# Optimization experiments

Hardware: AMD Instinct MI355X
Metric: run time of the kernel (lower is better)

Reference implementation:

```python
import jax, jax.numpy as jnp
import numpy as np

T, B, E, H = 256, 8, 512, 32
EXP = 512            # number of expanded (periodic-image) keys
SMOOTH = 20.0        # smooth_factor


def setup_inputs() -> dict:
    key = jax.random.key(0)
    ks = jax.random.split(key, 12)
    s = 1.0 / np.sqrt(E)
    return {
        "query": jax.random.normal(ks[0], (T, B, E), dtype=jnp.float32),
        "outcell_index": jax.random.randint(ks[1], (B, EXP), 0, T),
        "expand_mask": jax.random.bernoulli(ks[2], 0.1, (B, EXP)),
        "key_padding_mask": jax.random.bernoulli(ks[3], 0.1, (B, T)),
        "local_attention_weight": jax.random.uniform(ks[4], (B, T, T + EXP), dtype=jnp.float32),
        "Wq": jax.random.normal(ks[5], (E, E), dtype=jnp.float32) * s,
        "bq": jnp.zeros((E,), dtype=jnp.float32),
        "Wk": jax.random.normal(ks[6], (E, E), dtype=jnp.float32) * s,   # k_bias=False
        "Wv": jax.random.normal(ks[7], (E, E), dtype=jnp.float32) * s,
        "bv": jnp.zeros((E,), dtype=jnp.float32),
        "Wo": jax.random.normal(ks[8], (E, E), dtype=jnp.float32) * s,
        "bo": jnp.zeros((E,), dtype=jnp.float32),
    }


def reference(query, outcell_index, expand_mask, key_padding_mask,
              local_attention_weight, Wq, bq, Wk, Wv, bv, Wo, bo):
    t, b, e = query.shape
    hd = e // H
    # QKV projections (torch Linear: y = x @ W.T + b)
    q = jnp.einsum('tbe,fe->tbf', query, Wq) + bq
    k = jnp.einsum('tbe,fe->tbf', query, Wk)          # no k bias
    v = jnp.einsum('tbe,fe->tbf', query, Wv) + bv
    # PBC gather-expand K/V along the time axis
    oc = outcell_index.T[:, :, None]                  # [EXP, B, 1]
    k = jnp.concatenate([k, jnp.take_along_axis(k, oc, axis=0)], axis=0)  # [S,B,E]
    v = jnp.concatenate([v, jnp.take_along_axis(v, oc, axis=0)], axis=0)
    s_len = k.shape[0]
    # [len, B, E] -> [B, H, len, hd]
    qh = q.reshape(t, b, H, hd).transpose(1, 2, 0, 3)
    kh = k.reshape(s_len, b, H, hd).transpose(1, 2, 0, 3)
    vh = v.reshape(s_len, b, H, hd).transpose(1, 2, 0, 3)
    # NOTE: forward() never applies self.scaling in this path (faithful)
    scores = jnp.einsum('bhtd,bhsd->bhts', qh, kh)    # [B,H,T,S]
    law = local_attention_weight[:, None]             # [B,1,T,S]
    scores = (scores + SMOOTH) * law - SMOOTH         # smooth softmax
    kpm = jnp.concatenate([key_padding_mask, expand_mask], axis=1)  # [B,S]
    scores = jnp.where(kpm[:, None, None, :], -jnp.inf, scores)
    probs = jax.nn.softmax(scores, axis=-1)
    probs = probs * law                               # post-softmax reweight
    attn = jnp.einsum('bhts,bhsd->bhtd', probs, vh)   # [B,H,T,hd]
    attn = attn.transpose(2, 0, 1, 3).reshape(t, b, e)
    return jnp.einsum('tbe,fe->tbf', attn, Wo) + bo
```

## Files before the change

kernel.cpp:

```cpp
#include <hip/hip_runtime.h>
#include <stdint.h>

#define T_ 256
#define B_ 8
#define E_ 512
#define H_ 32
#define HD_ 16
#define EXP_ 512
#define S_ 768
#define M_ 2048
#define SMOOTH_ 20.0f
#define KSTR 20
#define VSTR 776
#define OSTR 20
#define LOG2E_ 1.44269504f
#define MB0_  (-100.988655f)

typedef __attribute__((ext_vector_type(8)))  short bf16x8;
typedef __attribute__((ext_vector_type(4)))  float f32x4;
typedef __attribute__((ext_vector_type(16))) float f32x16;
typedef __attribute__((ext_vector_type(2)))  unsigned int uint32x2;

__device__ __forceinline__ unsigned int cvtpk(float a, float b)
{
    unsigned int r;
    asm("v_cvt_pk_bf16_f32 %0, %1, %2" : "=v"(r) : "v"(a), "v"(b));
    return r;
}
__device__ __forceinline__ ushort bf1(float a)
{
    unsigned int u = __float_as_uint(a);
    u = u + 0x7FFFu + ((u >> 16) & 1u);
    return (ushort)(u >> 16);
}

union U16 { uint4 u; bf16x8 v; };
union U8x2 { uint2 p[2]; bf16x8 v; };

__device__ __forceinline__ bf16x8 ld20(const ushort* base, int row, int hi)
{
    U8x2 u;
    const ushort* p = &base[row * KSTR + hi * 8];
    u.p[0] = *(const uint2*)(p);
    u.p[1] = *(const uint2*)(p + 4);
    return u.v;
}

__global__ __launch_bounds__(1024, 4)
void qkv_attn_kernel(const float* __restrict__ X,
                     const float* __restrict__ Wq, const float* __restrict__ Wk,
                     const float* __restrict__ Wv,
                     const float* __restrict__ bq, const float* __restrict__ bv,
                     const float* __restrict__ LAW,
                     const int* __restrict__ kpm, const int* __restrict__ em,
                     const int* __restrict__ oc, ushort* __restrict__ Ab)
{
    __shared__ __align__(16) char raw[87552];
    ushort* Ks  = (ushort*)(raw);
    ushort* Vt  = (ushort*)(raw + 30720);
    ushort* Qi  = (ushort*)(raw + 55552);
    float*  msf = (float*) (raw + 65792);
    float*  Obuf= (float*) (raw);
    float*  Zb  = (float*) (raw + 65792);
    ushort* Ob  = Qi;

    const int bh  = blockIdx.x;
    const int b   = bh & 7;
    const int h   = bh >> 3;
    const int tid = threadIdx.x;
    const int w   = tid >> 6;
    const int l   = tid & 63;

    const int r0 = tid >> 3;
    const int c8 = tid & 7;
    const float* Xc0 = &X[((size_t)r0 * 8 + b) * E_ + c8 * 8];
    const float* Xc1 = Xc0 + (size_t)128 * 8 * E_;

    const int wr = tid >> 3;
    const bool wload = (tid < 384);
    const float* Wsel = (wr < 16) ? Wq : (wr < 32 ? Wk : Wv);
    const float* Wr = &Wsel[((size_t)(h * 16 + (wr & 15))) * E_ + c8 * 8];

    f32x4 acc[3];
#pragma unroll
    for (int m = 0; m < 3; ++m) acc[m] = (f32x4){0.f, 0.f, 0.f, 0.f};

    float4 xa0, xa1, xb0, xb1, wp0, wp1;
    xa0 = *(const float4*)&Xc0[0]; xa1 = *(const float4*)&Xc0[4];
    xb0 = *(const float4*)&Xc1[0]; xb1 = *(const float4*)&Xc1[4];
    if (wload) { wp0 = *(const float4*)&Wr[0]; wp1 = *(const float4*)&Wr[4]; }

    const int ln = l & 15;
    const int lg = l >> 4;

    for (int it = 0; it < 8; ++it) {
        ushort* Ad = (ushort*)(raw + (it & 1) * 43776);
        ushort* Bd = Ad + 18432;
        *(uint4*)&Ad[r0 * 72 + c8 * 8] =
            make_uint4(cvtpk(xa0.x, xa0.y), cvtpk(xa0.z, xa0.w),
                       cvtpk(xa1.x, xa1.y), cvtpk(xa1.z, xa1.w));
        *(uint4*)&Ad[(r0 + 128) * 72 + c8 * 8] =
            make_uint4(cvtpk(xb0.x, xb0.y), cvtpk(xb0.z, xb0.w),
                       cvtpk(xb1.x, xb1.y), cvtpk(xb1.z, xb1.w));
        if (wload)
            *(uint4*)&Bd[wr * 72 + c8 * 8] =
                make_uint4(cvtpk(wp0.x, wp0.y), cvtpk(wp0.z, wp0.w),
                           cvtpk(wp1.x, wp1.y), cvtpk(wp1.z, wp1.w));
        __syncthreads();
        if (it < 7) {
            Xc0 += 64; Xc1 += 64;
            xa0 = *(const float4*)&Xc0[0]; xa1 = *(const float4*)&Xc0[4];
            xb0 = *(const float4*)&Xc1[0]; xb1 = *(const float4*)&Xc1[4];
            if (wload) { Wr += 64; wp0 = *(const float4*)&Wr[0]; wp1 = *(const float4*)&Wr[4]; }
        }
#pragma unroll
        for (int kb = 0; kb < 2; ++kb) {
            bf16x8 af = *(const bf16x8*)&Ad[(w * 16 + ln) * 72 + kb * 32 + lg * 8];
#pragma unroll
            for (int m = 0; m < 3; ++m) {
                bf16x8 bfm = *(const bf16x8*)&Bd[(m * 16 + ln) * 72 + kb * 32 + lg * 8];
                acc[m] = __builtin_amdgcn_mfma_f32_16x16x32_bf16(af, bfm, acc[m], 0, 0, 0);
            }
        }
    }

    __syncthreads();

    {
        const float bqv = bq[h * 16 + ln];
        const float bvv = bv[h * 16 + ln];
#pragma unroll
        for (int r = 0; r < 4; ++r) {
            const int t = w * 16 + lg * 4 + r;
            Qi[t * KSTR + ln] = bf1(acc[0][r] + bqv);
            Ks[t * KSTR + ln] = bf1(acc[1][r]);
            Vt[ln * VSTR + t] = bf1(acc[2][r] + bvv);
        }
    }
    __syncthreads();

    if (tid < 512) {
        const int j   = tid;
        const int src = oc[b * EXP_ + j];
        const ushort* sp = &Ks[src * KSTR];
        ushort* dp = &Ks[(T_ + j) * KSTR];
        uint2 k0 = *(const uint2*)(sp);
        uint2 k1 = *(const uint2*)(sp + 4);
        uint2 k2 = *(const uint2*)(sp + 8);
        uint2 k3 = *(const uint2*)(sp + 12);
        uint2 k4 = *(const uint2*)(sp + 16);
        *(uint2*)(dp)      = k0;
        *(uint2*)(dp + 4)  = k1;
        *(uint2*)(dp + 8)  = k2;
        *(uint2*)(dp + 12) = k3;
        *(uint2*)(dp + 16) = k4;
    } else {
        const int j   = tid - 512;
        const int src = oc[b * EXP_ + j];
#pragma unroll
        for (int d = 0; d < 16; ++d)
            Vt[d * VSTR + T_ + j] = Vt[d * VSTR + src];
    }
    if (tid < 768) {
        const int s = tid;
        const int m = (s < T_) ? kpm[b * T_ + s] : em[b * EXP_ + (s - T_)];
        msf[s] = m ? -1.0e5f : MB0_;
    }
    __syncthreads();

    const int slane = l & 31;
    const int hi    = l >> 5;
    const int tq    = w & 7;
    const int sh    = w >> 3;
    const int i0    = sh * 12;
    const int iend  = i0 + 12;

    bf16x8 qf = ld20(Qi, tq * 32 + slane, hi);

    const f32x16 zero16 = {0.f,0.f,0.f,0.f,0.f,0.f,0.f,0.f,
                           0.f,0.f,0.f,0.f,0.f,0.f,0.f,0.f};
    f32x16 oacc = zero16;
    float zp0 = 0.f, zp1 = 0.f, zp2 = 0.f, zp3 = 0.f;

    const float* lawb = &LAW[((size_t)b * T_ + tq * 32 + slane) * S_ + 4 * hi];

    bf16x8 kf = ld20(Ks, i0 * 32 + slane, hi);
    float4 g0 = *(const float4*)&lawb[i0 * 32];
    float4 g1 = *(const float4*)&lawb[i0 * 32 + 8];
    float4 g2 = *(const float4*)&lawb[i0 * 32 + 16];
    float4 g3 = *(const float4*)&lawb[i0 * 32 + 24];

#pragma unroll 2
    for (int i = i0; i < iend; ++i) {
        const int inx = (i + 1 < iend) ? (i + 1) : i0;

        bf16x8 vf0 = *(const bf16x8*)&Vt[(l & 15) * VSTR + i * 32 + hi * 8];
        bf16x8 vf1 = *(const bf16x8*)&Vt[(l & 15) * VSTR + i * 32 + 16 + hi * 8];
        const float4 m0 = *(const float4*)&msf[i * 32 + 4 * hi];
        const float4 m1 = *(const float4*)&msf[i * 32 + 8 + 4 * hi];
        const float4 m2 = *(const float4*)&msf[i * 32 + 16 + 4 * hi];
        const float4 m3 = *(const float4*)&msf[i * 32 + 24 + 4 * hi];

        f32x16 sc = __builtin_amdgcn_mfma_f32_32x32x16_bf16(kf, qf, zero16, 0, 0, 0);

        bf16x8 kfn = ld20(Ks, inx * 32 + slane, hi);

        const float4 lwg[4] = {g0, g1, g2, g3};
        const float4 mbg[4] = {m0, m1, m2, m3};

#pragma unroll
        for (int ks = 0; ks < 2; ++ks) {
            float pp[8];
#pragma unroll
            for (int gi = 0; gi < 2; ++gi) {
                const int g = 2 * ks + gi;
                const float4 lw4 = lwg[g];
                const float4 mb4 = mbg[g];
                const float lwa[4] = {lw4.x, lw4.y, lw4.z, lw4.w};
                const float mba[4] = {mb4.x, mb4.y, mb4.z, mb4.w};
#pragma unroll
                for (int c = 0; c < 4; ++c) {
                    const float lwv = lwa[c];
                    const float lwK = lwv * LOG2E_;
                    const float arg = __builtin_fmaf(sc[8 * ks + 4 * gi + c], lwK,
                                      __builtin_fmaf(lwK, SMOOTH_, mba[c]));
                    const float e = __builtin_amdgcn_exp2f(arg);
                    if (c == 0) zp0 += e; else if (c == 1) zp1 += e;
                    else if (c == 2) zp2 += e; else zp3 += e;
                    pp[4 * gi + c] = e * lwv;
                }
            }
            const unsigned int cA0 = cvtpk(pp[0], pp[1]);
            const unsigned int cA2 = cvtpk(pp[2], pp[3]);
            const unsigned int cB0 = cvtpk(pp[4], pp[5]);
            const unsigned int cB2 = cvtpk(pp[6], pp[7]);
            uint32x2 s0 = __builtin_amdgcn_permlane32_swap(cA0, cB0, false, false);
            uint32x2 s1 = __builtin_amdgcn_permlane32_swap(cA2, cB2, false, false);
            U16 u;
            u.u = make_uint4(s0.x, s1.x, s0.y, s1.y);
            oacc = __builtin_amdgcn_mfma_f32_32x32x16_bf16(
                       u.v, ks ? vf1 : vf0, oacc, 0, 0, 0);
        }

        g0 = *(const float4*)&lawb[inx * 32];
        g1 = *(const float4*)&lawb[inx * 32 + 8];
        g2 = *(const float4*)&lawb[inx * 32 + 16];
        g3 = *(const float4*)&lawb[inx * 32 + 24];
        kf = kfn;
    }

    float z = (zp0 + zp1) + (zp2 + zp3);
    z += __shfl_xor(z, 32);

    __syncthreads();

    if (l < 32) Zb[sh * 256 + tq * 32 + l] = z;

    const int dl = l & 15;
    const bool dok = (l & 31) < 16;
    if (sh == 1 && dok) {
#pragma unroll
        for (int r = 0; r < 16; ++r) {
            const int t = tq * 32 + (r & 3) + 8 * (r >> 2) + 4 * hi;
            Obuf[t * OSTR + dl] = oacc[r];
        }
    }
    __syncthreads();

    if (sh == 0 && dok) {
#pragma unroll
        for (int r = 0; r < 16; ++r) {
            const int t = tq * 32 + (r & 3) + 8 * (r >> 2) + 4 * hi;
            const float Zt  = Zb[t] + Zb[256 + t];
            const float inv = (Zt > 0.f) ? 1.f / Zt : 0.f;
            const float ov  = (oacc[r] + Obuf[t * OSTR + dl]) * inv;
            Ob[t * 16 + dl] = bf1(ov);
        }
    }
    __syncthreads();

    {
        const int t  = tid >> 2;
        const int q4 = tid & 3;
        *(uint2*)&Ab[((size_t)(t * 8 + b)) * E_ + h * 16 + q4 * 4] =
            *(const uint2*)&Ob[t * 16 + q4 * 4];
    }
}

__global__ __launch_bounds__(256, 2)
void out_gemm(const ushort* __restrict__ Ab, const float* __restrict__ Wo,
              const float* __restrict__ bo, float* __restrict__ dst)
{
    __shared__ __align__(16) ushort sbuf[96 * 136];
    ushort* As = sbuf;
    ushort* Bs = sbuf + 32 * 136;

    const int n0 = blockIdx.x * 64;
    const int m0 = blockIdx.y * 32;

    const int tid = threadIdx.x;
    const int arow = tid >> 3;
    const int acol = (tid & 7) * 16;
    const int brow = tid >> 2;
    const int bcol = (tid & 3) * 32;

    const ushort* Ap = &Ab[(size_t)(m0 + arow) * E_ + acol];
    const float*  Wp = &Wo[(size_t)(n0 + brow) * E_ + bcol];

    f32x4 acc[2];
    acc[0] = (f32x4){0.f, 0.f, 0.f, 0.f};
    acc[1] = (f32x4){0.f, 0.f, 0.f, 0.f};

    uint4  ha0 = *(const uint4*)&Ap[0];
    uint4  ha1 = *(const uint4*)&Ap[8];
    float4 f0 = *(const float4*)&Wp[0];
    float4 f1 = *(const float4*)&Wp[4];
    float4 f2 = *(const float4*)&Wp[8];
    float4 f3 = *(const float4*)&Wp[12];
    float4 f4 = *(const float4*)&Wp[16];
    float4 f5 = *(const float4*)&Wp[20];
    float4 f6 = *(const float4*)&Wp[24];
    float4 f7 = *(const float4*)&Wp[28];

    const int l  = tid & 63;
    const int w  = tid >> 6;
    const int wm = w & 1;
    const int wn = w >> 1;
    const int lq = l >> 4;
    const int ln = l & 15;

    for (int it = 0; it < 4; ++it) {
        __syncthreads();
        *(uint4*)&As[arow * 136 + acol]     = ha0;
        *(uint4*)&As[arow * 136 + acol + 8] = ha1;
        *(uint4*)&Bs[brow * 136 + bcol]      = make_uint4(cvtpk(f0.x, f0.y), cvtpk(f0.z, f0.w),
                                                          cvtpk(f1.x, f1.y), cvtpk(f1.z, f1.w));
        *(uint4*)&Bs[brow * 136 + bcol + 8]  = make_uint4(cvtpk(f2.x, f2.y), cvtpk(f2.z, f2.w),
                                                          cvtpk(f3.x, f3.y), cvtpk(f3.z, f3.w));
        *(uint4*)&Bs[brow * 136 + bcol + 16] = make_uint4(cvtpk(f4.x, f4.y), cvtpk(f4.z, f4.w),
                                                          cvtpk(f5.x, f5.y), cvtpk(f5.z, f5.w));
        *(uint4*)&Bs[brow * 136 + bcol + 24] = make_uint4(cvtpk(f6.x, f6.y), cvtpk(f6.z, f6.w),
                                                          cvtpk(f7.x, f7.y), cvtpk(f7.z, f7.w));
        __syncthreads();
        if (it < 3) {
            Ap += 128; Wp += 128;
            ha0 = *(const uint4*)&Ap[0];
            ha1 = *(const uint4*)&Ap[8];
            f0 = *(const float4*)&Wp[0];
            f1 = *(const float4*)&Wp[4];
            f2 = *(const float4*)&Wp[8];
            f3 = *(const float4*)&Wp[12];
            f4 = *(const float4*)&Wp[16];
            f5 = *(const float4*)&Wp[20];
            f6 = *(const float4*)&Wp[24];
            f7 = *(const float4*)&Wp[28];
        }
#pragma unroll
        for (int kb = 0; kb < 4; ++kb) {
            bf16x8 af  = *(const bf16x8*)&As[(wm * 16 + ln) * 136 + kb * 32 + lq * 8];
            bf16x8 bv0 = *(const bf16x8*)&Bs[(wn * 32 + ln) * 136 + kb * 32 + lq * 8];
            bf16x8 bv1 = *(const bf16x8*)&Bs[(wn * 32 + 16 + ln) * 136 + kb * 32 + lq * 8];
            acc[0] = __builtin_amdgcn_mfma_f32_16x16x32_bf16(af, bv0, acc[0], 0, 0, 0);
            acc[1] = __builtin_amdgcn_mfma_f32_16x16x32_bf16(af, bv1, acc[1], 0, 0, 0);
        }
    }

    const float bo0 = bo[n0 + wn * 32 + ln];
    const float bo1 = bo[n0 + wn * 32 + 16 + ln];

    __syncthreads();
    float* Lf = (float*)sbuf;
#pragma unroll
    for (int j = 0; j < 2; ++j) {
        const float bb = j ? bo1 : bo0;
        const f32x4 a = acc[j];
#pragma unroll
        for (int r = 0; r < 4; ++r)
            Lf[(wm * 16 + lq * 4 + r) * 68 + wn * 32 + j * 16 + ln] = a[r] + bb;
    }
    __syncthreads();

    {
        const int orow = tid >> 3;
        const int oc8  = (tid & 7) * 8;
        float* dp = &dst[(size_t)(m0 + orow) * E_ + n0 + oc8];
        float4 v0 = *(const float4*)&Lf[orow * 68 + oc8];
        float4 v1 = *(const float4*)&Lf[orow * 68 + oc8 + 4];
        *(float4*)&dp[0] = v0;
        *(float4*)&dp[4] = v1;
    }
}

extern "C" void kernel_launch(void* const* d_in, const int* in_sizes, int n_in,
                              void* d_out, int out_size, void* d_ws, size_t ws_size,
                              hipStream_t stream)
{
    const float* query = (const float*)d_in[0];
    const int*   oc    = (const int*)d_in[1];
    const int*   em    = (const int*)d_in[2];
    const int*   kpm   = (const int*)d_in[3];
    const float* law   = (const float*)d_in[4];
    const float* Wq    = (const float*)d_in[5];
    const float* bq    = (const float*)d_in[6];
    const float* Wk    = (const float*)d_in[7];
    const float* Wv    = (const float*)d_in[8];
    const float* bv    = (const float*)d_in[9];
    const float* Wo    = (const float*)d_in[10];
    const float* bo    = (const float*)d_in[11];
    float* out = (float*)d_out;

    ushort* Ab = (ushort*)d_ws;

    qkv_attn_kernel<<<B_ * H_, 1024, 0, stream>>>(query, Wq, Wk, Wv, bq, bv,
                                                  law, kpm, em, oc, Ab);

    dim3 go(E_ / 64, M_ / 32, 1);
    out_gemm<<<go, 256, 0, stream>>>(Ab, Wo, bo, out);
}
```

Baseline: 131.1 us.

## Split fused QKV+attention kernel into projection and split-key attention kernels

The single fused kernel (one 1024-thread block per batch-head) becomes two kernels. A projection kernel writes Q, gathered K and V^T to workspace. An attention kernel then launches two 512-thread blocks per batch-head, each covering half the key range, and writes unnormalised partial outputs and softmax denominators. The output GEMM now merges the two halves, normalises and converts to bf16 while loading its A tile. This doubles the block count and shrinks shared memory per block to raise occupancy, at the cost of extra global round trips for K/V/Q and fp32 partials, plus one more kernel launch.

```diff
diff --git a/kernel.cpp b/kernel.cpp
--- a/kernel.cpp
+++ b/kernel.cpp
@@ -12,7 +12,7 @@
 #define SMOOTH_ 20.0f
 #define KSTR 20
 #define VSTR 776
-#define OSTR 20
+#define VTH  392
 #define LOG2E_ 1.44269504f
 #define MB0_  (-100.988655f)
 
@@ -47,22 +47,18 @@
 }
 
 __global__ __launch_bounds__(1024, 4)
-void qkv_attn_kernel(const float* __restrict__ X,
-                     const float* __restrict__ Wq, const float* __restrict__ Wk,
-                     const float* __restrict__ Wv,
-                     const float* __restrict__ bq, const float* __restrict__ bv,
-                     const float* __restrict__ LAW,
-                     const int* __restrict__ kpm, const int* __restrict__ em,
-                     const int* __restrict__ oc, ushort* __restrict__ Ab)
+void qkv_proj(const float* __restrict__ X,
+              const float* __restrict__ Wq, const float* __restrict__ Wk,
+              const float* __restrict__ Wv,
+              const float* __restrict__ bq, const float* __restrict__ bv,
+              const int* __restrict__ oc,
+              ushort* __restrict__ wsK, ushort* __restrict__ wsV,
+              ushort* __restrict__ wsQ)
 {
     __shared__ __align__(16) char raw[87552];
     ushort* Ks  = (ushort*)(raw);
     ushort* Vt  = (ushort*)(raw + 30720);
     ushort* Qi  = (ushort*)(raw + 55552);
-    float*  msf = (float*) (raw + 65792);
-    float*  Obuf= (float*) (raw);
-    float*  Zb  = (float*) (raw + 65792);
-    ushort* Ob  = Qi;
 
     const int bh  = blockIdx.x;
     const int b   = bh & 7;
@@ -148,12 +144,10 @@
         uint2 k1 = *(const uint2*)(sp + 4);
         uint2 k2 = *(const uint2*)(sp + 8);
         uint2 k3 = *(const uint2*)(sp + 12);
-        uint2 k4 = *(const uint2*)(sp + 16);
         *(uint2*)(dp)      = k0;
         *(uint2*)(dp + 4)  = k1;
         *(uint2*)(dp + 8)  = k2;
         *(uint2*)(dp + 12) = k3;
-        *(uint2*)(dp + 16) = k4;
     } else {
         const int j   = tid - 512;
         const int src = oc[b * EXP_ + j];
@@ -161,19 +155,103 @@
         for (int d = 0; d < 16; ++d)
             Vt[d * VSTR + T_ + j] = Vt[d * VSTR + src];
     }
+    __syncthreads();
+
     if (tid < 768) {
-        const int s = tid;
+        const ushort* sp = &Ks[tid * KSTR];
+        uint2 a0 = *(const uint2*)(sp);
+        uint2 a1 = *(const uint2*)(sp + 4);
+        uint2 a2 = *(const uint2*)(sp + 8);
+        uint2 a3 = *(const uint2*)(sp + 12);
+        ushort* gp = &wsK[((size_t)bh * 768 + tid) * 16];
+        *(uint4*)(gp)     = make_uint4(a0.x, a0.y, a1.x, a1.y);
+        *(uint4*)(gp + 8) = make_uint4(a2.x, a2.y, a3.x, a3.y);
+    } else {
+        const int r = tid - 768;
+        const ushort* sp = &Qi[r * KSTR];
+        uint2 a0 = *(const uint2*)(sp);
+        uint2 a1 = *(const uint2*)(sp + 4);
+        uint2 a2 = *(const uint2*)(sp + 8);
+        uint2 a3 = *(const uint2*)(sp + 12);
+        ushort* gp = &wsQ[((size_t)bh * 256 + r) * 16];
+        *(uint4*)(gp)     = make_uint4(a0.x, a0.y, a1.x, a1.y);
+        *(uint4*)(gp + 8) = make_uint4(a2.x, a2.y, a3.x, a3.y);
+    }
+    {
+        const int d = tid >> 6;
+        const int c = tid & 63;
+        const ushort* sp = &Vt[d * VSTR + c * 12];
+        uint2 v0 = *(const uint2*)(sp);
+        uint2 v1 = *(const uint2*)(sp + 4);
+        uint2 v2 = *(const uint2*)(sp + 8);
+        ushort* gp = &wsV[(size_t)bh * 16 * 768 + d * 768 + c * 12];
+        *(uint2*)(gp)     = v0;
+        *(uint2*)(gp + 4) = v1;
+        *(uint2*)(gp + 8) = v2;
+    }
+}
+
+__global__ __launch_bounds__(512, 4)
+void attn_half(const float* __restrict__ LAW,
+               const int* __restrict__ kpm, const int* __restrict__ em,
+               const ushort* __restrict__ wsK, const ushort* __restrict__ wsV,
+               const ushort* __restrict__ wsQ,
+               float* __restrict__ wsO, float* __restrict__ wsZ)
+{
+    __shared__ __align__(16) char raw[39680];
+    ushort* Qi  = (ushort*)(raw);
+    ushort* Ksh = (ushort*)(raw + 10240);
+    ushort* Vth = (ushort*)(raw + 25600);
+    float*  msf = (float*) (raw + 38144);
+
+    const int bid = blockIdx.x;
+    const int bh  = bid >> 1;
+    const int sh  = bid & 1;
+    const int b   = bh & 7;
+    const int h   = bh >> 3;
+    const int tid = threadIdx.x;
+    const int w   = tid >> 6;
+    const int l   = tid & 63;
+
+    {
+        const ushort* QgB = &wsQ[(size_t)bh * 256 * 16];
+        const int r  = tid >> 1;
+        const int hf = tid & 1;
+        uint4 q = *(const uint4*)&QgB[r * 16 + hf * 8];
+        ushort* qp = &Qi[r * KSTR + hf * 8];
+        *(uint2*)(qp)     = make_uint2(q.x, q.y);
+        *(uint2*)(qp + 4) = make_uint2(q.z, q.w);
+    }
+    if (tid < 384) {
+        const ushort* kp = &wsK[((size_t)bh * 768 + sh * 384 + tid) * 16];
+        uint4 k0 = *(const uint4*)(kp);
+        uint4 k1 = *(const uint4*)(kp + 8);
+        ushort* dp = &Ksh[tid * KSTR];
+        *(uint2*)(dp)      = make_uint2(k0.x, k0.y);
+        *(uint2*)(dp + 4)  = make_uint2(k0.z, k0.w);
+        *(uint2*)(dp + 8)  = make_uint2(k1.x, k1.y);
+        *(uint2*)(dp + 12) = make_uint2(k1.z, k1.w);
+        const int s = sh * 384 + tid;
         const int m = (s < T_) ? kpm[b * T_ + s] : em[b * EXP_ + (s - T_)];
-        msf[s] = m ? -1.0e5f : MB0_;
+        msf[tid] = m ? -1.0e5f : MB0_;
+    }
+    {
+        const int d = tid >> 5;
+        const int c = tid & 31;
+        const ushort* vp = &wsV[(size_t)bh * 16 * 768 + d * 768 + sh * 384 + c * 12];
+        uint2 v0 = *(const uint2*)(vp);
+        uint2 v1 = *(const uint2*)(vp + 4);
+        uint2 v2 = *(const uint2*)(vp + 8);
+        ushort* dp = &Vth[d * VTH + c * 12];
+        *(uint2*)(dp)     = v0;
+        *(uint2*)(dp + 4) = v1;
+        *(uint2*)(dp + 8) = v2;
     }
     __syncthreads();
 
     const int slane = l & 31;
     const int hi    = l >> 5;
-    const int tq    = w & 7;
-    const int sh    = w >> 3;
-    const int i0    = sh * 12;
-    const int iend  = i0 + 12;
+    const int tq    = w;
 
     bf16x8 qf = ld20(Qi, tq * 32 + slane, hi);
 
@@ -183,27 +261,28 @@
     float zp0 = 0.f, zp1 = 0.f, zp2 = 0.f, zp3 = 0.f;
 
     const float* lawb = &LAW[((size_t)b * T_ + tq * 32 + slane) * S_ + 4 * hi];
-
-    bf16x8 kf = ld20(Ks, i0 * 32 + slane, hi);
-    float4 g0 = *(const float4*)&lawb[i0 * 32];
-    float4 g1 = *(const float4*)&lawb[i0 * 32 + 8];
-    float4 g2 = *(const float4*)&lawb[i0 * 32 + 16];
-    float4 g3 = *(const float4*)&lawb[i0 * 32 + 24];
+    const int ig0 = sh * 12;
+
+    bf16x8 kf = ld20(Ksh, slane, hi);
+    float4 g0 = *(const float4*)&lawb[ig0 * 32];
+    float4 g1 = *(const float4*)&lawb[ig0 * 32 + 8];
+    float4 g2 = *(const float4*)&lawb[ig0 * 32 + 16];
+    float4 g3 = *(const float4*)&lawb[ig0 * 32 + 24];
 
 #pragma unroll 2
-    for (int i = i0; i < iend; ++i) {
-        const int inx = (i + 1 < iend) ? (i + 1) : i0;
-
-        bf16x8 vf0 = *(const bf16x8*)&Vt[(l & 15) * VSTR + i * 32 + hi * 8];
-        bf16x8 vf1 = *(const bf16x8*)&Vt[(l & 15) * VSTR + i * 32 + 16 + hi * 8];
-        const float4 m0 = *(const float4*)&msf[i * 32 + 4 * hi];
-        const float4 m1 = *(const float4*)&msf[i * 32 + 8 + 4 * hi];
-        const float4 m2 = *(const float4*)&msf[i * 32 + 16 + 4 * hi];
-        const float4 m3 = *(const float4*)&msf[i * 32 + 24 + 4 * hi];
+    for (int ii = 0; ii < 12; ++ii) {
+        const int iin = (ii + 1 < 12) ? (ii + 1) : 0;
+
+        bf16x8 vf0 = *(const bf16x8*)&Vth[(l & 15) * VTH + ii * 32 + hi * 8];
+        bf16x8 vf1 = *(const bf16x8*)&Vth[(l & 15) * VTH + ii * 32 + 16 + hi * 8];
+        const float4 m0 = *(const float4*)&msf[ii * 32 + 4 * hi];
+        const float4 m1 = *(const float4*)&msf[ii * 32 + 8 + 4 * hi];
+        const float4 m2 = *(const float4*)&msf[ii * 32 + 16 + 4 * hi];
+        const float4 m3 = *(const float4*)&msf[ii * 32 + 24 + 4 * hi];
 
         f32x16 sc = __builtin_amdgcn_mfma_f32_32x32x16_bf16(kf, qf, zero16, 0, 0, 0);
 
-        bf16x8 kfn = ld20(Ks, inx * 32 + slane, hi);
+        bf16x8 kfn = ld20(Ksh, iin * 32 + slane, hi);
 
         const float4 lwg[4] = {g0, g1, g2, g3};
         const float4 mbg[4] = {m0, m1, m2, m3};
@@ -242,54 +321,36 @@
                        u.v, ks ? vf1 : vf0, oacc, 0, 0, 0);
         }
 
-        g0 = *(const float4*)&lawb[inx * 32];
-        g1 = *(const float4*)&lawb[inx * 32 + 8];
-        g2 = *(const float4*)&lawb[inx * 32 + 16];
-        g3 = *(const float4*)&lawb[inx * 32 + 24];
+        const int ign = ig0 + iin;
+        g0 = *(const float4*)&lawb[ign * 32];
+        g1 = *(const float4*)&lawb[ign * 32 + 8];
+        g2 = *(const float4*)&lawb[ign * 32 + 16];
+        g3 = *(const float4*)&lawb[ign * 32 + 24];
         kf = kfn;
     }
 
     float z = (zp0 + zp1) + (zp2 + zp3);
     z += __shfl_xor(z, 32);
 
-    __syncthreads();
-
-    if (l < 32) Zb[sh * 256 + tq * 32 + l] = z;
-
-    const int dl = l & 15;
-    const bool dok = (l & 31) < 16;
-    if (sh == 1 && dok) {
+    if ((l & 31) < 16) {
+        const int dl = l & 15;
+        float* Op = &wsO[(size_t)sh * M_ * E_ + (size_t)h * 16 + dl];
 #pragma unroll
         for (int r = 0; r < 16; ++r) {
             const int t = tq * 32 + (r & 3) + 8 * (r >> 2) + 4 * hi;
-            Obuf[t * OSTR + dl] = oacc[r];
-        }
-    }
-    __syncthreads();
-
-    if (sh == 0 && dok) {
-#pragma unroll
-        for (int r = 0; r < 16; ++r) {
-            const int t = tq * 32 + (r & 3) + 8 * (r >> 2) + 4 * hi;
-            const float Zt  = Zb[t] + Zb[256 + t];
-            const float inv = (Zt > 0.f) ? 1.f / Zt : 0.f;
-            const float ov  = (oacc[r] + Obuf[t * OSTR + dl]) * inv;
-            Ob[t * 16 + dl] = bf1(ov);
-        }
-    }
-    __syncthreads();
-
-    {
-        const int t  = tid >> 2;
-        const int q4 = tid & 3;
-        *(uint2*)&Ab[((size_t)(t * 8 + b)) * E_ + h * 16 + q4 * 4] =
-            *(const uint2*)&Ob[t * 16 + q4 * 4];
+            Op[(size_t)(t * 8 + b) * E_] = oacc[r];
+        }
+    }
+    if (l < 32) {
+        const int t = tq * 32 + l;
+        wsZ[(size_t)sh * M_ * H_ + ((size_t)(t * 8 + b)) * H_ + h] = z;
     }
 }
 
 __global__ __launch_bounds__(256, 2)
-void out_gemm(const ushort* __restrict__ Ab, const float* __restrict__ Wo,
-              const float* __restrict__ bo, float* __restrict__ dst)
+void out_gemm(const float* __restrict__ wsO, const float* __restrict__ wsZ,
+              const float* __restrict__ Wo, const float* __restrict__ bo,
+              float* __restrict__ dst)
 {
     __shared__ __align__(16) ushort sbuf[96 * 136];
     ushort* As = sbuf;
@@ -304,15 +365,25 @@
     const int brow = tid >> 2;
     const int bcol = (tid & 3) * 32;
 
-    const ushort* Ap = &Ab[(size_t)(m0 + arow) * E_ + acol];
+    const float* O0p = &wsO[(size_t)(m0 + arow) * E_ + acol];
+    const float* O1p = O0p + (size_t)M_ * E_;
+    const float* Zp  = &wsZ[(size_t)(m0 + arow) * H_];
+    const float* Z1p = Zp + (size_t)M_ * H_;
     const float*  Wp = &Wo[(size_t)(n0 + brow) * E_ + bcol];
 
     f32x4 acc[2];
     acc[0] = (f32x4){0.f, 0.f, 0.f, 0.f};
     acc[1] = (f32x4){0.f, 0.f, 0.f, 0.f};
 
-    uint4  ha0 = *(const uint4*)&Ap[0];
-    uint4  ha1 = *(const uint4*)&Ap[8];
+    float4 oa0 = *(const float4*)&O0p[0];
+    float4 oa1 = *(const float4*)&O0p[4];
+    float4 oa2 = *(const float4*)&O0p[8];
+    float4 oa3 = *(const float4*)&O0p[12];
+    float4 ob0 = *(const float4*)&O1p[0];
+    float4 ob1 = *(const float4*)&O1p[4];
+    float4 ob2 = *(const float4*)&O1p[8];
+    float4 ob3 = *(const float4*)&O1p[12];
+    float  zs  = Zp[acol >> 4] + Z1p[acol >> 4];
     float4 f0 = *(const float4*)&Wp[0];
     float4 f1 = *(const float4*)&Wp[4];
     float4 f2 = *(const float4*)&Wp[8];
@@ -331,8 +402,21 @@
 
     for (int it = 0; it < 4; ++it) {
         __syncthreads();
-        *(uint4*)&As[arow * 136 + acol]     = ha0;
-        *(uint4*)&As[arow * 136 + acol + 8] = ha1;
+        {
+            const float inv = (zs > 0.f) ? 1.f / zs : 0.f;
+            const float c0 = (oa0.x + ob0.x) * inv, c1 = (oa0.y + ob0.y) * inv;
+            const float c2 = (oa0.z + ob0.z) * inv, c3 = (oa0.w + ob0.w) * inv;
+            const float c4 = (oa1.x + ob1.x) * inv, c5 = (oa1.y + ob1.y) * inv;
+            const float c6 = (oa1.z + ob1.z) * inv, c7 = (oa1.w + ob1.w) * inv;
+            const float c8 = (oa2.x + ob2.x) * inv, c9 = (oa2.y + ob2.y) * inv;
+            const float ca = (oa2.z + ob2.z) * inv, cb = (oa2.w + ob2.w) * inv;
+            const float cc = (oa3.x + ob3.x) * inv, cd = (oa3.y + ob3.y) * inv;
+            const float ce = (oa3.z + ob3.z) * inv, cf = (oa3.w + ob3.w) * inv;
+            *(uint4*)&As[arow * 136 + acol] =
+                make_uint4(cvtpk(c0, c1), cvtpk(c2, c3), cvtpk(c4, c5), cvtpk(c6, c7));
+            *(uint4*)&As[arow * 136 + acol + 8] =
+                make_uint4(cvtpk(c8, c9), cvtpk(ca, cb), cvtpk(cc, cd), cvtpk(ce, cf));
+        }
         *(uint4*)&Bs[brow * 136 + bcol]      = make_uint4(cvtpk(f0.x, f0.y), cvtpk(f0.z, f0.w),
                                                           cvtpk(f1.x, f1.y), cvtpk(f1.z, f1.w));
         *(uint4*)&Bs[brow * 136 + bcol + 8]  = make_uint4(cvtpk(f2.x, f2.y), cvtpk(f2.z, f2.w),
@@ -343,9 +427,16 @@
                                                           cvtpk(f7.x, f7.y), cvtpk(f7.z, f7.w));
         __syncthreads();
         if (it < 3) {
-            Ap += 128; Wp += 128;
-            ha0 = *(const uint4*)&Ap[0];
-            ha1 = *(const uint4*)&Ap[8];
+            O0p += 128; O1p += 128; Wp += 128;
+            oa0 = *(const float4*)&O0p[0];
+            oa1 = *(const float4*)&O0p[4];
+            oa2 = *(const float4*)&O0p[8];
+            oa3 = *(const float4*)&O0p[12];
+            ob0 = *(const float4*)&O1p[0];
+            ob1 = *(const float4*)&O1p[4];
+            ob2 = *(const float4*)&O1p[8];
+            ob3 = *(const float4*)&O1p[12];
+            zs  = Zp[(it + 1) * 8 + (acol >> 4)] + Z1p[(it + 1) * 8 + (acol >> 4)];
             f0 = *(const float4*)&Wp[0];
             f1 = *(const float4*)&Wp[4];
             f2 = *(const float4*)&Wp[8];
@@ -409,11 +500,19 @@
     const float* bo    = (const float*)d_in[11];
     float* out = (float*)d_out;
 
-    ushort* Ab = (ushort*)d_ws;
-
-    qkv_attn_kernel<<<B_ * H_, 1024, 0, stream>>>(query, Wq, Wk, Wv, bq, bv,
-                                                  law, kpm, em, oc, Ab);
+    char* ws = (char*)d_ws;
+    ushort* wsK = (ushort*)(ws);
+    ushort* wsV = (ushort*)(ws + 6291456);
+    ushort* wsQ = (ushort*)(ws + 12582912);
+    float*  wsO = (float*) (ws + 14680064);
+    float*  wsZ = (float*) (ws + 23068672);
+
+    qkv_proj<<<B_ * H_, 1024, 0, stream>>>(query, Wq, Wk, Wv, bq, bv, oc,
+                                           wsK, wsV, wsQ);
+
+    attn_half<<<B_ * H_ * 2, 512, 0, stream>>>(law, kpm, em, wsK, wsV, wsQ,
+                                               wsO, wsZ);
 
     dim3 go(E_ / 64, M_ / 32, 1);
-    out_gemm<<<go, 256, 0, stream>>>(Ab, Wo, bo, out);
-}
+    out_gemm<<<go, 256, 0, stream>>>(wsO, wsZ, Wo, bo, out);
+}
```

Result: slower. 146.5 us (+11.7%).
